# Kernel tuning notes

Measured on AMD Instinct MI355X. Metric: run time of the kernel, lower is better.

Reference implementation:

```python
import jax, jax.numpy as jnp
import numpy as np

N, E = 50000, 800000          # nodes, directed edges
F_IN = 80                     # 16 unique sensors * 5 features
H, C = 4, 96                  # num_heads, hidden_dim
D = H * C                     # 384 = concat output dim per GAT layer
NC = 20                       # n_classes = number of components
NEG_SLOPE = 0.2               # PyG GATv2Conv default negative_slope
EPS = 1e-5                    # LayerNorm eps


def layer_norm(x, g, b):
    mu = x.mean(-1, keepdims=True)
    var = x.var(-1, keepdims=True)
    return (x - mu) * jax.lax.rsqrt(var + EPS) * g + b


def gatv2(x, src, dst, Wsrc, Wdst, att, bias):
    # GATv2Conv (concat=True): e_ij = att . leaky_relu(Wsrc x_j + Wdst x_i),
    # alpha = segment-softmax over dst, out_i = sum_j alpha_ij * (Wsrc x_j)
    n = x.shape[0]
    xs = (x @ Wsrc).reshape(n, H, C)
    xd = (x @ Wdst).reshape(n, H, C)
    m = jax.nn.leaky_relu(xs[src] + xd[dst], NEG_SLOPE)      # [E,H,C]
    e = jnp.einsum('ehc,hc->eh', m, att)                     # [E,H]
    emax = jax.ops.segment_max(e, dst, num_segments=n)       # [N,H]
    ex = jnp.exp(e - emax[dst])
    denom = jax.ops.segment_sum(ex, dst, num_segments=n)
    alpha = ex / (denom[dst] + 1e-16)                        # [E,H]
    out = jax.ops.segment_sum(alpha[:, :, None] * xs[src], dst, num_segments=n)
    return out.reshape(n, D) + bias


def setup_inputs():
    key = jax.random.key(0)
    ks = jax.random.split(key, 16)

    def w(k, shape, fan):
        return (jax.random.normal(k, shape, jnp.float32) / np.float32(np.sqrt(fan)))

    inp = {
        'x': jax.random.normal(ks[0], (N, F_IN), jnp.float32),
        'edge_index': jax.random.randint(ks[1], (2, E), 0, N, jnp.int32),
    }
    dims = [F_IN, D, D]
    i = 2
    for l in range(3):
        inp[f'Wsrc{l}'] = w(ks[i], (dims[l], D), dims[l]); i += 1
        inp[f'Wdst{l}'] = w(ks[i], (dims[l], D), dims[l]); i += 1
        inp[f'att{l}'] = w(ks[i], (H, C), C); i += 1
        inp[f'b{l}'] = jnp.zeros((D,), jnp.float32)
        inp[f'g{l}'] = jnp.ones((D,), jnp.float32)
        inp[f'be{l}'] = jnp.zeros((D,), jnp.float32)
    inp['Wc1'] = w(ks[i], (D, C), D); i += 1
    inp['bc1'] = jnp.zeros((C,), jnp.float32)
    inp['gc'] = jnp.ones((C,), jnp.float32)
    inp['bec'] = jnp.zeros((C,), jnp.float32)
    inp['Wc2'] = w(ks[i], (C, NC), C)
    inp['bc2'] = jnp.zeros((NC,), jnp.float32)
    return inp


def reference(x, edge_index,
              Wsrc0, Wdst0, att0, b0, g0, be0,
              Wsrc1, Wdst1, att1, b1, g1, be1,
              Wsrc2, Wdst2, att2, b2, g2, be2,
              Wc1, bc1, gc, bec, Wc2, bc2):
    src, dst = edge_index[0], edge_index[1]
    layers = [(Wsrc0, Wdst0, att0, b0, g0, be0),
              (Wsrc1, Wdst1, att1, b1, g1, be1),
              (Wsrc2, Wdst2, att2, b2, g2, be2)]
    h = x
    for (Ws, Wd, a, b, g, be) in layers:
        h = gatv2(h, src, dst, Ws, Wd, a, b)
        h = jax.nn.elu(layer_norm(h, g, be))   # dropout: identity in eval mode
    h = jax.nn.relu(h @ Wc1 + bc1)
    h = layer_norm(h, gc, bec)
    return h @ Wc2 + bc2
```

## Files before the change

kernel.cpp:

```cpp
#include <hip/hip_runtime.h>
#include <math.h>

#define D 384
#define NCLS 20
#define FIN 80
#define CH 96

typedef unsigned int u32t;
typedef unsigned short u16t;
typedef __attribute__((ext_vector_type(8))) short bf16x8;
typedef __attribute__((ext_vector_type(4))) float f32x4;

__device__ __forceinline__ u16t f2bf(float f) {
    u32t b = __float_as_uint(f);
    u32t r = (b + 0x7FFFu + ((b >> 16) & 1u)) >> 16;
    return (u16t)r;
}
__device__ __forceinline__ float bfl(u32t u) { return __uint_as_float(u << 16); }
__device__ __forceinline__ float bfh(u32t u) { return __uint_as_float(u & 0xFFFF0000u); }

#define GLOAD16(g, l)                                                            \
    __builtin_amdgcn_global_load_lds(                                            \
        (const __attribute__((address_space(1))) void*)(g),                      \
        (__attribute__((address_space(3))) void*)(l), 16, 0, 0)


__global__ void k_zero(int* p, int n) {
    int i = blockIdx.x * blockDim.x + threadIdx.x;
    if (i < n) p[i] = 0;
}

__global__ void k_hist(const int* __restrict__ dst, int* __restrict__ deg, int E) {
    int i = blockIdx.x * blockDim.x + threadIdx.x;
    if (i < E) atomicAdd(&deg[dst[i]], 1);
}

__global__ __launch_bounds__(256) void k_scan1(const int* __restrict__ deg,
                                               int* __restrict__ offs,
                                               int* __restrict__ bsum, int n) {
    __shared__ int sh[256];
    int t = threadIdx.x, i = blockIdx.x * 256 + t;
    int v = (i < n) ? deg[i] : 0;
    sh[t] = v;
    __syncthreads();
    for (int o = 1; o < 256; o <<= 1) {
        int a = (t >= o) ? sh[t - o] : 0;
        __syncthreads();
        sh[t] += a;
        __syncthreads();
    }
    if (i < n) offs[i] = sh[t] - v;
    if (t == 255) bsum[blockIdx.x] = sh[255];
}

__global__ __launch_bounds__(256) void k_scan2(int* __restrict__ bsum, int nb,
                                               int* __restrict__ offs, int n) {
    __shared__ int sh[256];
    int t = threadIdx.x;
    int v = (t < nb) ? bsum[t] : 0;
    sh[t] = v;
    __syncthreads();
    for (int o = 1; o < 256; o <<= 1) {
        int a = (t >= o) ? sh[t - o] : 0;
        __syncthreads();
        sh[t] += a;
        __syncthreads();
    }
    if (t < nb) bsum[t] = sh[t] - v;
    if (t == 255) offs[n] = sh[255];
}

__global__ __launch_bounds__(256) void k_scan3(int* __restrict__ offs,
                                               int* __restrict__ cursor,
                                               const int* __restrict__ bsum, int n) {
    int i = blockIdx.x * 256 + threadIdx.x;
    if (i < n) {
        int o = offs[i] + bsum[blockIdx.x];
        offs[i] = o;
        cursor[i] = o;
    }
}

__global__ void k_scatter(const int* __restrict__ src, const int* __restrict__ dst,
                          int* __restrict__ cursor, int* __restrict__ csr_srcb, int E) {
    int i = blockIdx.x * blockDim.x + threadIdx.x;
    if (i < E) {
        int p = atomicAdd(&cursor[dst[i]], 1);
        csr_srcb[p] = src[i] * 384;
    }
}


__global__ __launch_bounds__(256) void k_cvt_all(
    const float* __restrict__ x,
    const float* __restrict__ Ws0, const float* __restrict__ Wd0,
    const float* __restrict__ Ws1, const float* __restrict__ Wd1,
    const float* __restrict__ Ws2, const float* __restrict__ Wd2,
    const float* __restrict__ Wc1,
    u16t* __restrict__ xbf,
    u16t* __restrict__ WT0s, u16t* __restrict__ WT0d,
    u16t* __restrict__ WT1s, u16t* __restrict__ WT1d,
    u16t* __restrict__ WT2s, u16t* __restrict__ WT2d,
    u16t* __restrict__ Wc1T, int N) {
    const int s96 = 384 * 96, s384 = 384 * 384, sc1 = 128 * 384;
    int i = blockIdx.x * 256 + threadIdx.x;

    int n0 = N * 96;
    if (i < n0) {
        int r = i / 96, c = i - r * 96;
        xbf[i] = f2bf(c < FIN ? x[r * FIN + c] : 0.f);
        return;
    }
    i -= n0;
    if (i < 2 * s96) {
        const float* W = (i < s96) ? Ws0 : Wd0;
        u16t* O = (i < s96) ? WT0s : WT0d;
        int k2 = (i < s96) ? i : i - s96;
        int c = k2 / 96, k = k2 - c * 96;
        O[k2] = f2bf(k < FIN ? W[(size_t)k * D + c] : 0.f);
        return;
    }
    i -= 2 * s96;
    if (i < 4 * s384) {
        int w = i / s384, k2 = i - w * s384;
        const float* W = (w == 0) ? Ws1 : (w == 1) ? Wd1 : (w == 2) ? Ws2 : Wd2;
        u16t* O = (w == 0) ? WT1s : (w == 1) ? WT1d : (w == 2) ? WT2s : WT2d;
        int c = k2 / 384, k = k2 - c * 384;
        O[k2] = f2bf(W[(size_t)k * D + c]);
        return;
    }
    i -= 4 * s384;
    if (i < sc1) {
        int c = i / D, k = i - c * D;
        Wc1T[i] = f2bf(c < CH ? Wc1[(size_t)k * CH + c] : 0.f);
    }
}


__global__ __launch_bounds__(256) void k_mm(const u16t* __restrict__ A,
                                            const u16t* __restrict__ BT,
                                            u16t* __restrict__ C, int Kp, int ostride) {
    __shared__ u16t Al[4][128][8];
    __shared__ u16t Bl[4][128][8];
    const int t = threadIdx.x;
    const int wave = t >> 6, lane = t & 63;
    const int wr = wave >> 1, wc = wave & 1;
    const int bm0 = blockIdx.x * 128;
    const int bn0 = blockIdx.y * 128;
    const int col16 = lane & 15, kc = lane >> 4;

    f32x4 acc[4][4] = {};

    const u16t* asrc0 = A + (size_t)(bm0 + lane) * Kp + wave * 8;
    const u16t* asrc1 = A + (size_t)(bm0 + 64 + lane) * Kp + wave * 8;
    const u16t* bsrc0 = BT + (size_t)(bn0 + lane) * Kp + wave * 8;
    const u16t* bsrc1 = BT + (size_t)(bn0 + 64 + lane) * Kp + wave * 8;
    u16t* alds0 = &Al[wave][0][0];
    u16t* alds1 = &Al[wave][64][0];
    u16t* blds0 = &Bl[wave][0][0];
    u16t* blds1 = &Bl[wave][64][0];

    for (int k0 = 0; k0 < Kp; k0 += 32) {
        GLOAD16(asrc0 + k0, alds0);
        GLOAD16(asrc1 + k0, alds1);
        GLOAD16(bsrc0 + k0, blds0);
        GLOAD16(bsrc1 + k0, blds1);
        __syncthreads();

        bf16x8 a[4], b[4];
#pragma unroll
        for (int m = 0; m < 4; m++)
            a[m] = *(const bf16x8*)&Al[kc][wr * 64 + m * 16 + col16][0];
#pragma unroll
        for (int n = 0; n < 4; n++)
            b[n] = *(const bf16x8*)&Bl[kc][wc * 64 + n * 16 + col16][0];
#pragma unroll
        for (int m = 0; m < 4; m++)
#pragma unroll
            for (int n = 0; n < 4; n++)
                acc[m][n] = __builtin_amdgcn_mfma_f32_16x16x32_bf16(
                    a[m], b[n], acc[m][n], 0, 0, 0);
        __syncthreads();
    }

#pragma unroll
    for (int m = 0; m < 4; m++) {
#pragma unroll
        for (int n = 0; n < 4; n++) {
#pragma unroll
            for (int j = 0; j < 4; j++) {
                int row = bm0 + wr * 64 + m * 16 + (lane >> 4) * 4 + j;
                int col = bn0 + wc * 64 + n * 16 + col16;
                C[(size_t)row * ostride + col] = f2bf(acc[m][n][j]);
            }
        }
    }
}


__global__ __launch_bounds__(256) void k_mmh(const u16t* __restrict__ A,
                                             const u16t* __restrict__ BT,
                                             const float* __restrict__ bc1,
                                             float* __restrict__ Yh) {
    __shared__ u16t Al[4][128][8];
    __shared__ u16t Bl[4][128][8];
    const int t = threadIdx.x;
    const int wave = t >> 6, lane = t & 63;
    const int wr = wave >> 1, wc = wave & 1;
    const int bm0 = blockIdx.x * 128;
    const int col16 = lane & 15, kc = lane >> 4;

    f32x4 acc[4][4] = {};

    const u16t* asrc0 = A + (size_t)(bm0 + lane) * D + wave * 8;
    const u16t* asrc1 = A + (size_t)(bm0 + 64 + lane) * D + wave * 8;
    const u16t* bsrc0 = BT + (size_t)lane * D + wave * 8;
    const u16t* bsrc1 = BT + (size_t)(64 + lane) * D + wave * 8;
    u16t* alds0 = &Al[wave][0][0];
    u16t* alds1 = &Al[wave][64][0];
    u16t* blds0 = &Bl[wave][0][0];
    u16t* blds1 = &Bl[wave][64][0];

    for (int k0 = 0; k0 < D; k0 += 32) {
        GLOAD16(asrc0 + k0, alds0);
        GLOAD16(asrc1 + k0, alds1);
        GLOAD16(bsrc0 + k0, blds0);
        GLOAD16(bsrc1 + k0, blds1);
        __syncthreads();

        bf16x8 a[4], b[4];
#pragma unroll
        for (int m = 0; m < 4; m++)
            a[m] = *(const bf16x8*)&Al[kc][wr * 64 + m * 16 + col16][0];
#pragma unroll
        for (int n = 0; n < 4; n++)
            b[n] = *(const bf16x8*)&Bl[kc][wc * 64 + n * 16 + col16][0];
#pragma unroll
        for (int m = 0; m < 4; m++)
#pragma unroll
            for (int n = 0; n < 4; n++)
                acc[m][n] = __builtin_amdgcn_mfma_f32_16x16x32_bf16(
                    a[m], b[n], acc[m][n], 0, 0, 0);
        __syncthreads();
    }

#pragma unroll
    for (int m = 0; m < 4; m++) {
#pragma unroll
        for (int n = 0; n < 4; n++) {
            int col = wc * 64 + n * 16 + col16;
            if (col < CH) {
                float bc = bc1[col];
#pragma unroll
                for (int j = 0; j < 4; j++) {
                    int row = bm0 + wr * 64 + m * 16 + (lane >> 4) * 4 + j;
                    Yh[(size_t)row * CH + col] = fmaxf(acc[m][n][j] + bc, 0.f);
                }
            }
        }
    }
}


__global__ __launch_bounds__(256) void k_gat(const u32t* __restrict__ XSXD,
                                             const float* __restrict__ att,
                                             const float* __restrict__ bias,
                                             const float* __restrict__ gamma,
                                             const float* __restrict__ beta,
                                             const int* __restrict__ offs,
                                             const int* __restrict__ csr_srcb,
                                             u16t* __restrict__ Hout,
                                             int N) {
    int wave = threadIdx.x >> 6;
    int lane = threadIdx.x & 63;
    int node = blockIdx.x * 4 + wave;
    if (node >= N) return;
    int c0 = lane * 6;
    int lo3 = lane * 3;

    const u32t* xdp = XSXD + (size_t)node * 384 + 192 + lo3;
    u32t d0 = xdp[0], d1 = xdp[1], d2 = xdp[2];
    float xd[6] = {bfl(d0), bfh(d0), bfl(d1), bfh(d1), bfl(d2), bfh(d2)};
    float attr[6];
#pragma unroll
    for (int k = 0; k < 6; k++) attr[k] = att[c0 + k] * 1.44269504f;

    float m = -INFINITY, denom = 0.f;
    float acc[6] = {0.f, 0.f, 0.f, 0.f, 0.f, 0.f};
    int e0 = offs[node], e1 = offs[node + 1];

    for (int base = e0; base < e1; base += 64) {
        int cnt = min(64, e1 - base);
        u32t midx = (lane < cnt) ? (u32t)csr_srcb[base + lane] : 0u;
        u32t off = __builtin_amdgcn_readlane(midx, 0);
        const u32t* p = XSXD + off + lo3;
        u32t a0 = p[0], a1 = p[1], a2 = p[2];

        for (int j = 0; j < cnt; j++) {
            u32t b0 = a0, b1 = a1, b2 = a2;
            if (j + 1 < cnt) {
                u32t offn = __builtin_amdgcn_readlane(midx, j + 1);
                const u32t* pn = XSXD + offn + lo3;
                a0 = pn[0]; a1 = pn[1]; a2 = pn[2];
            }
            float xs[6] = {bfl(b0), bfh(b0), bfl(b1), bfh(b1), bfl(b2), bfh(b2)};
            float part = 0.f;
#pragma unroll
            for (int k = 0; k < 6; k++) {
                float v = xs[k] + xd[k];
                part = fmaf(fmaxf(v, 0.2f * v), attr[k], part);
            }
#pragma unroll
            for (int o = 1; o < 16; o <<= 1) part += __shfl_xor(part, o, 64);

            if (__builtin_expect(__any(part - m > 8.0f), 0)) {
                float nm = fmaxf(m, part);
                float r = __builtin_amdgcn_exp2f(m - nm);
                float pp = __builtin_amdgcn_exp2f(part - nm);
                denom = denom * r + pp;
#pragma unroll
                for (int k = 0; k < 6; k++) acc[k] = fmaf(pp, xs[k], acc[k] * r);
                m = nm;
            } else {
                float pp = __builtin_amdgcn_exp2f(part - m);
                denom += pp;
#pragma unroll
                for (int k = 0; k < 6; k++) acc[k] = fmaf(pp, xs[k], acc[k]);
            }
        }
    }

    float inv = 1.f / (denom + 1e-16f);
    float v[6];
    float s1 = 0.f;
#pragma unroll
    for (int k = 0; k < 6; k++) { v[k] = acc[k] * inv + bias[c0 + k]; s1 += v[k]; }
#pragma unroll
    for (int o = 1; o < 64; o <<= 1) s1 += __shfl_xor(s1, o, 64);
    float mu = s1 * (1.f / 384.f);
    float s2 = 0.f;
#pragma unroll
    for (int k = 0; k < 6; k++) { float d = v[k] - mu; s2 += d * d; }
#pragma unroll
    for (int o = 1; o < 64; o <<= 1) s2 += __shfl_xor(s2, o, 64);
    float rstd = rsqrtf(s2 * (1.f / 384.f) + 1e-5f);

    float ov[6];
#pragma unroll
    for (int k = 0; k < 6; k++) {
        float y = (v[k] - mu) * rstd * gamma[c0 + k] + beta[c0 + k];
        ov[k] = y > 0.f ? y : __expf(y) - 1.f;
    }
    u32t w0 = (u32t)f2bf(ov[0]) | ((u32t)f2bf(ov[1]) << 16);
    u32t w1 = (u32t)f2bf(ov[2]) | ((u32t)f2bf(ov[3]) << 16);
    u32t w2 = (u32t)f2bf(ov[4]) | ((u32t)f2bf(ov[5]) << 16);
    u32t* hp = (u32t*)Hout + (size_t)node * 192 + lo3;
    hp[0] = w0; hp[1] = w1; hp[2] = w2;
}


__global__ __launch_bounds__(256) void k_lnout(const float* __restrict__ Yh,
                                               const float* __restrict__ gc,
                                               const float* __restrict__ bec,
                                               const float* __restrict__ Wc2,
                                               const float* __restrict__ bc2,
                                               float* __restrict__ out, int N) {
    __shared__ float w2[CH * NCLS];
    __shared__ float ln[8][CH];
    int t = threadIdx.x;
    int g = t >> 5, tl = t & 31;
    int node = blockIdx.x * 8 + g;

    for (int i = t; i < CH * NCLS; i += 256) w2[i] = Wc2[i];

    if (node < N) {
        const float* yp = Yh + (size_t)node * CH;
        float y0 = yp[tl], y1 = yp[32 + tl], y2 = yp[64 + tl];
        float s = y0 + y1 + y2;
#pragma unroll
        for (int o = 1; o < 32; o <<= 1) s += __shfl_xor(s, o, 32);
        float mu = s * (1.f / CH);
        float d0 = y0 - mu, d1 = y1 - mu, d2 = y2 - mu;
        float q = d0 * d0 + d1 * d1 + d2 * d2;
#pragma unroll
        for (int o = 1; o < 32; o <<= 1) q += __shfl_xor(q, o, 32);
        float rstd = rsqrtf(q * (1.f / CH) + 1e-5f);
        ln[g][tl]      = d0 * rstd * gc[tl]      + bec[tl];
        ln[g][32 + tl] = d1 * rstd * gc[32 + tl] + bec[32 + tl];
        ln[g][64 + tl] = d2 * rstd * gc[64 + tl] + bec[64 + tl];
    }
    __syncthreads();

    if (node < N && tl < NCLS) {
        float o = bc2[tl];
        for (int c = 0; c < CH; c++) o += ln[g][c] * w2[c * NCLS + tl];
        out[(size_t)node * NCLS + tl] = o;
    }
}


extern "C" void kernel_launch(void* const* d_in, const int* in_sizes, int n_in,
                              void* d_out, int out_size, void* d_ws, size_t ws_size,
                              hipStream_t stream) {
    const float* x        = (const float*)d_in[0];
    const int*   eidx     = (const int*)d_in[1];
    const float* Wsrc[3]  = {(const float*)d_in[2],  (const float*)d_in[8],  (const float*)d_in[14]};
    const float* Wdst[3]  = {(const float*)d_in[3],  (const float*)d_in[9],  (const float*)d_in[15]};
    const float* attw[3]  = {(const float*)d_in[4],  (const float*)d_in[10], (const float*)d_in[16]};
    const float* bia[3]   = {(const float*)d_in[5],  (const float*)d_in[11], (const float*)d_in[17]};
    const float* gam[3]   = {(const float*)d_in[6],  (const float*)d_in[12], (const float*)d_in[18]};
    const float* bet[3]   = {(const float*)d_in[7],  (const float*)d_in[13], (const float*)d_in[19]};
    const float* Wc1 = (const float*)d_in[20];
    const float* bc1 = (const float*)d_in[21];
    const float* gc  = (const float*)d_in[22];
    const float* bec = (const float*)d_in[23];
    const float* Wc2 = (const float*)d_in[24];
    const float* bc2 = (const float*)d_in[25];

    const int N = in_sizes[0] / FIN;
    const int E = in_sizes[1] / 2;
    const int Mpad = ((N + 127) / 128) * 128;
    const int* srcp = eidx;
    const int* dstp = eidx + E;

    u16t* xbf  = (u16t*)d_ws;
    u16t* XSXD = xbf + (size_t)Mpad * 96;
    u16t* Hbf  = XSXD + (size_t)Mpad * 768;
    u16t* WT0s = Hbf + (size_t)Mpad * D;
    u16t* WT0d = WT0s + 384 * 96;
    u16t* WT1s = WT0d + 384 * 96;
    u16t* WT1d = WT1s + 384 * 384;
    u16t* WT2s = WT1d + 384 * 384;
    u16t* WT2d = WT2s + 384 * 384;
    u16t* Wc1T = WT2d + 384 * 384;
    float* Yh  = (float*)(Wc1T + 128 * 384);
    int* offs    = (int*)(Yh + (size_t)Mpad * CH);
    int* cursor  = offs + (N + 1);
    int* deg     = cursor + (N + 1);
    int* bsum    = deg + N;
    int* csr_srcb = bsum + 512;

    const int nb = (N + 255) / 256;

    k_zero<<<nb, 256, 0, stream>>>(deg, N);
    k_hist<<<(E + 255) / 256, 256, 0, stream>>>(dstp, deg, E);
    k_scan1<<<nb, 256, 0, stream>>>(deg, offs, bsum, N);
    k_scan2<<<1, 256, 0, stream>>>(bsum, nb, offs, N);
    k_scan3<<<nb, 256, 0, stream>>>(offs, cursor, bsum, N);
    k_scatter<<<(E + 255) / 256, 256, 0, stream>>>(srcp, dstp, cursor, csr_srcb, E);

    {
        long total = (long)N * 96 + 2L * (384 * 96) + 4L * (384 * 384) + 128L * 384;
        int cblocks = (int)((total + 255) / 256);
        k_cvt_all<<<cblocks, 256, 0, stream>>>(
            x, Wsrc[0], Wdst[0], Wsrc[1], Wdst[1], Wsrc[2], Wdst[2], Wc1,
            xbf, WT0s, WT0d, WT1s, WT1d, WT2s, WT2d, Wc1T, N);
    }

    dim3 gmm(Mpad / 128, 768 / 128);
    int gatGrid = (N + 3) / 4;

    k_mm<<<gmm, 256, 0, stream>>>(xbf, WT0s, XSXD, 96, 768);
    k_gat<<<gatGrid, 256, 0, stream>>>((const u32t*)XSXD, attw[0], bia[0], gam[0], bet[0],
                                       offs, csr_srcb, Hbf, N);
    k_mm<<<gmm, 256, 0, stream>>>(Hbf, WT1s, XSXD, D, 768);
    k_gat<<<gatGrid, 256, 0, stream>>>((const u32t*)XSXD, attw[1], bia[1], gam[1], bet[1],
                                       offs, csr_srcb, Hbf, N);
    k_mm<<<gmm, 256, 0, stream>>>(Hbf, WT2s, XSXD, D, 768);
    k_gat<<<gatGrid, 256, 0, stream>>>((const u32t*)XSXD, attw[2], bia[2], gam[2], bet[2],
                                       offs, csr_srcb, Hbf, N);

    k_mmh<<<Mpad / 128, 256, 0, stream>>>(Hbf, Wc1T, bc1, Yh);
    k_lnout<<<(N + 7) / 8, 256, 0, stream>>>(Yh, gc, bec, Wc2, bc2,
                                             (float*)d_out, N);
}
```

Before: 749.8 us.

## Fuse classifier head, swap GEMM grid order, shrink GAT blocks, memset degrees

```diff
diff --git a/kernel.cpp b/kernel.cpp
--- a/kernel.cpp
+++ b/kernel.cpp
@@ -24,11 +24,6 @@
         (const __attribute__((address_space(1))) void*)(g),                      \
         (__attribute__((address_space(3))) void*)(l), 16, 0, 0)
 
-
-__global__ void k_zero(int* p, int n) {
-    int i = blockIdx.x * blockDim.x + threadIdx.x;
-    if (i < n) p[i] = 0;
-}
 
 __global__ void k_hist(const int* __restrict__ dst, int* __restrict__ deg, int E) {
     int i = blockIdx.x * blockDim.x + threadIdx.x;
@@ -145,8 +140,8 @@
     const int t = threadIdx.x;
     const int wave = t >> 6, lane = t & 63;
     const int wr = wave >> 1, wc = wave & 1;
-    const int bm0 = blockIdx.x * 128;
-    const int bn0 = blockIdx.y * 128;
+    const int bm0 = blockIdx.y * 128;
+    const int bn0 = blockIdx.x * 128;
     const int col16 = lane & 15, kc = lane >> 4;
 
     f32x4 acc[4][4] = {};
@@ -198,17 +193,25 @@
 }
 
 
-__global__ __launch_bounds__(256) void k_mmh(const u16t* __restrict__ A,
-                                             const u16t* __restrict__ BT,
-                                             const float* __restrict__ bc1,
-                                             float* __restrict__ Yh) {
+__global__ __launch_bounds__(256) void k_headf(const u16t* __restrict__ A,
+                                               const u16t* __restrict__ BT,
+                                               const float* __restrict__ bc1,
+                                               const float* __restrict__ gc,
+                                               const float* __restrict__ bec,
+                                               const float* __restrict__ Wc2,
+                                               const float* __restrict__ bc2,
+                                               float* __restrict__ out, int N) {
     __shared__ u16t Al[4][128][8];
     __shared__ u16t Bl[4][128][8];
+    __shared__ float ys[128][100];
+    __shared__ float w2s[CH * NCLS];
     const int t = threadIdx.x;
     const int wave = t >> 6, lane = t & 63;
     const int wr = wave >> 1, wc = wave & 1;
     const int bm0 = blockIdx.x * 128;
     const int col16 = lane & 15, kc = lane >> 4;
+
+    for (int i = t; i < CH * NCLS; i += 256) w2s[i] = Wc2[i];
 
     f32x4 acc[4][4] = {};
 
@@ -253,16 +256,42 @@
                 float bc = bc1[col];
 #pragma unroll
                 for (int j = 0; j < 4; j++) {
-                    int row = bm0 + wr * 64 + m * 16 + (lane >> 4) * 4 + j;
-                    Yh[(size_t)row * CH + col] = fmaxf(acc[m][n][j] + bc, 0.f);
+                    int row = wr * 64 + m * 16 + (lane >> 4) * 4 + j;
+                    ys[row][col] = fmaxf(acc[m][n][j] + bc, 0.f);
                 }
             }
         }
     }
-}
-
-
-__global__ __launch_bounds__(256) void k_gat(const u32t* __restrict__ XSXD,
+    __syncthreads();
+
+    int r = t >> 1, h = t & 1;
+    int node = bm0 + r;
+    float s = 0.f;
+    for (int c = h * 48; c < h * 48 + 48; c++) s += ys[r][c];
+    s += __shfl_xor(s, 1, 64);
+    float mu = s * (1.f / CH);
+    float q = 0.f;
+    for (int c = h * 48; c < h * 48 + 48; c++) { float d = ys[r][c] - mu; q += d * d; }
+    q += __shfl_xor(q, 1, 64);
+    float rstd = rsqrtf(q * (1.f / CH) + 1e-5f);
+    __syncthreads();
+    for (int c = h * 48; c < h * 48 + 48; c++)
+        ys[r][c] = (ys[r][c] - mu) * rstd * gc[c] + bec[c];
+    __syncthreads();
+
+    if (node < N) {
+#pragma unroll
+        for (int jj = 0; jj < NCLS / 2; jj++) {
+            int j = h * (NCLS / 2) + jj;
+            float o = bc2[j];
+            for (int c = 0; c < CH; c++) o = fmaf(ys[r][c], w2s[c * NCLS + j], o);
+            out[(size_t)node * NCLS + j] = o;
+        }
+    }
+}
+
+
+__global__ __launch_bounds__(128) void k_gat(const u32t* __restrict__ XSXD,
                                              const float* __restrict__ att,
                                              const float* __restrict__ bias,
                                              const float* __restrict__ gamma,
@@ -273,7 +302,7 @@
                                              int N) {
     int wave = threadIdx.x >> 6;
     int lane = threadIdx.x & 63;
-    int node = blockIdx.x * 4 + wave;
+    int node = blockIdx.x * 2 + wave;
     if (node >= N) return;
     int c0 = lane * 6;
     int lo3 = lane * 3;
@@ -356,46 +385,6 @@
     u32t w2 = (u32t)f2bf(ov[4]) | ((u32t)f2bf(ov[5]) << 16);
     u32t* hp = (u32t*)Hout + (size_t)node * 192 + lo3;
     hp[0] = w0; hp[1] = w1; hp[2] = w2;
-}
-
-
-__global__ __launch_bounds__(256) void k_lnout(const float* __restrict__ Yh,
-                                               const float* __restrict__ gc,
-                                               const float* __restrict__ bec,
-                                               const float* __restrict__ Wc2,
-                                               const float* __restrict__ bc2,
-                                               float* __restrict__ out, int N) {
-    __shared__ float w2[CH * NCLS];
-    __shared__ float ln[8][CH];
-    int t = threadIdx.x;
-    int g = t >> 5, tl = t & 31;
-    int node = blockIdx.x * 8 + g;
-
-    for (int i = t; i < CH * NCLS; i += 256) w2[i] = Wc2[i];
-
-    if (node < N) {
-        const float* yp = Yh + (size_t)node * CH;
-        float y0 = yp[tl], y1 = yp[32 + tl], y2 = yp[64 + tl];
-        float s = y0 + y1 + y2;
-#pragma unroll
-        for (int o = 1; o < 32; o <<= 1) s += __shfl_xor(s, o, 32);
-        float mu = s * (1.f / CH);
-        float d0 = y0 - mu, d1 = y1 - mu, d2 = y2 - mu;
-        float q = d0 * d0 + d1 * d1 + d2 * d2;
-#pragma unroll
-        for (int o = 1; o < 32; o <<= 1) q += __shfl_xor(q, o, 32);
-        float rstd = rsqrtf(q * (1.f / CH) + 1e-5f);
-        ln[g][tl]      = d0 * rstd * gc[tl]      + bec[tl];
-        ln[g][32 + tl] = d1 * rstd * gc[32 + tl] + bec[32 + tl];
-        ln[g][64 + tl] = d2 * rstd * gc[64 + tl] + bec[64 + tl];
-    }
-    __syncthreads();
-
-    if (node < N && tl < NCLS) {
-        float o = bc2[tl];
-        for (int c = 0; c < CH; c++) o += ln[g][c] * w2[c * NCLS + tl];
-        out[(size_t)node * NCLS + tl] = o;
-    }
 }
 
 
@@ -433,8 +422,7 @@
     u16t* WT2s = WT1d + 384 * 384;
     u16t* WT2d = WT2s + 384 * 384;
     u16t* Wc1T = WT2d + 384 * 384;
-    float* Yh  = (float*)(Wc1T + 128 * 384);
-    int* offs    = (int*)(Yh + (size_t)Mpad * CH);
+    int* offs    = (int*)(Wc1T + 128 * 384);
     int* cursor  = offs + (N + 1);
     int* deg     = cursor + (N + 1);
     int* bsum    = deg + N;
@@ -442,7 +430,7 @@
 
     const int nb = (N + 255) / 256;
 
-    k_zero<<<nb, 256, 0, stream>>>(deg, N);
+    hipMemsetAsync(deg, 0, (size_t)N * sizeof(int), stream);
     k_hist<<<(E + 255) / 256, 256, 0, stream>>>(dstp, deg, E);
     k_scan1<<<nb, 256, 0, stream>>>(deg, offs, bsum, N);
     k_scan2<<<1, 256, 0, stream>>>(bsum, nb, offs, N);
@@ -457,20 +445,19 @@
             xbf, WT0s, WT0d, WT1s, WT1d, WT2s, WT2d, Wc1T, N);
     }
 
-    dim3 gmm(Mpad / 128, 768 / 128);
-    int gatGrid = (N + 3) / 4;
+    dim3 gmm(768 / 128, Mpad / 128);
+    int gatGrid = (N + 1) / 2;
 
     k_mm<<<gmm, 256, 0, stream>>>(xbf, WT0s, XSXD, 96, 768);
-    k_gat<<<gatGrid, 256, 0, stream>>>((const u32t*)XSXD, attw[0], bia[0], gam[0], bet[0],
+    k_gat<<<gatGrid, 128, 0, stream>>>((const u32t*)XSXD, attw[0], bia[0], gam[0], bet[0],
                                        offs, csr_srcb, Hbf, N);
     k_mm<<<gmm, 256, 0, stream>>>(Hbf, WT1s, XSXD, D, 768);
-    k_gat<<<gatGrid, 256, 0, stream>>>((const u32t*)XSXD, attw[1], bia[1], gam[1], bet[1],
+    k_gat<<<gatGrid, 128, 0, stream>>>((const u32t*)XSXD, attw[1], bia[1], gam[1], bet[1],
                                        offs, csr_srcb, Hbf, N);
     k_mm<<<gmm, 256, 0, stream>>>(Hbf, WT2s, XSXD, D, 768);
-    k_gat<<<gatGrid, 256, 0, stream>>>((const u32t*)XSXD, attw[2], bia[2], gam[2], bet[2],
+    k_gat<<<gatGrid, 128, 0, stream>>>((const u32t*)XSXD, attw[2], bia[2], gam[2], bet[2],
                                        offs, csr_srcb, Hbf, N);
 
-    k_mmh<<<Mpad / 128, 256, 0, stream>>>(Hbf, Wc1T, bc1, Yh);
-    k_lnout<<<(N + 7) / 8, 256, 0, stream>>>(Yh, gc, bec, Wc2, bc2,
-                                             (float*)d_out, N);
-}
+    k_headf<<<Mpad / 128, 256, 0, stream>>>(Hbf, Wc1T, bc1, gc, bec, Wc2, bc2,
+                                            (float*)d_out, N);
+}
```

Result: no change. 760.0 us (+1.4%).
